# Kernel tuning notes

Hardware: AMD Instinct MI355X
Metric: run time of the kernel (lower is better)

The kernel has to match this reference:

```python
import jax, jax.numpy as jnp
import numpy as np

PATCH = (1, 5, 5)   # NN_patch_size (t, h, w)
CHUNK = 3600


def unfold3d_patches(video):
    """video: [B,C,T,H,W] -> [N, d] overlapping (1,5,5) patches, stride 1, VALID.
    d = C*1*5*5; N = B*T*(H-4)*(W-4). Element order within d is consistent
    across calls, which is all the L2 KNN + MSE math requires."""
    p = jax.lax.conv_general_dilated_patches(
        video, filter_shape=PATCH, window_strides=(1, 1, 1), padding='VALID')
    # p: [B, C*prod(PATCH), T', H', W']
    d = p.shape[1]
    return jnp.moveaxis(p, 1, -1).reshape(-1, d)


def knn_argmin(q, k):
    """Exact 1-NN under L2 (faiss IndexFlatL2 equivalent), chunked over queries."""
    kn = jnp.sum(k * k, axis=1)                      # [Nk]
    qc = q.reshape(-1, CHUNK, q.shape[1])            # [nchunks, CHUNK, d]

    def one_chunk(qb):
        qn = jnp.sum(qb * qb, axis=1, keepdims=True)  # [CHUNK,1]
        d2 = qn + kn[None, :] - 2.0 * (qb @ k.T)      # [CHUNK, Nk]
        return jnp.argmin(d2, axis=1)

    return jax.lax.map(one_chunk, qc).reshape(-1)    # [Nq]


def setup_inputs() -> dict:
    key = jax.random.key(0)
    k1, k2 = jax.random.split(key)
    shape = (1, 3, 4, 64, 64)  # [B,C,T,H,W]
    return {
        'result': jax.random.normal(k1, shape, dtype=jnp.float32),
        'valid_video': jax.random.normal(k2, shape, dtype=jnp.float32),
    }


def reference(result, valid_video):
    q = unfold3d_patches(result)        # [Nq, 75] query patches
    k = unfold3d_patches(valid_video)   # [Nk, 75] valid (key/value) patches
    idx = knn_argmin(q, k)              # [Nq] nearest valid patch per query
    nn = k[idx]                         # gather (F.embedding equivalent)
    # nn.MSELoss(reduction='sum')
    diff = q - nn
    return jnp.sum(diff * diff)
```

## Files before the change

### kernel.cpp

```cpp
#include <hip/hip_runtime.h>
#include <hip/hip_bf16.h>
#include <math.h>

typedef __attribute__((ext_vector_type(4))) float f32x4;
typedef __attribute__((ext_vector_type(2))) long long2_t;

#define NP 14400
#define NPK 14592
#define NSEG 16
#define NIT 57
#define GRPB 1536

__device__ __forceinline__ unsigned char f2fp8(float x) {
  unsigned u = __float_as_uint(x);
  unsigned sign = (u >> 31) << 7;
  int exp = (int)((u >> 23) & 0xFF) - 127;
  unsigned man = u & 0x7FFFFF;
  if (exp >= -6) {
    unsigned keep = man >> 20;
    unsigned rest = man & 0xFFFFF;
    keep += (rest > 0x80000u) || (rest == 0x80000u && (keep & 1));
    int e8 = exp + 7;
    if (keep == 8) { keep = 0; e8 += 1; }
    if (e8 > 15 || (e8 == 15 && keep == 7)) return sign | 0x7E;
    return sign | ((unsigned)e8 << 3) | keep;
  } else {
    float a = fabsf(x);
    int q = (int)(a * 512.f + 0.5f);
    if (q >= 8) return sign | 0x08;
    return sign | (unsigned)q;
  }
}
__device__ __forceinline__ float fp82f(unsigned char b) {
  unsigned e = (b >> 3) & 15, m = b & 7;
  float v = (e == 0) ? ldexpf((float)m, -9) : ldexpf((float)(8 + m), (int)e - 10);
  return (b & 0x80) ? -v : v;
}

__device__ __forceinline__ size_t f8idx(int p, int d) {
  int g = p >> 4, c = p & 15, ks = d >> 5, l4e = (d & 31) >> 3, e7 = d & 7;
  size_t base = (size_t)g * GRPB;
  if (ks < 2) return base + (size_t)((c + 16 * l4e) * 16 + ks * 8 + e7);
  return base + 1024 + (size_t)((c + 16 * l4e) * 8 + e7);
}

__global__ __launch_bounds__(256) void prep_kernel(
    const float* __restrict__ resv, const float* __restrict__ valv,
    unsigned char* __restrict__ Qb, unsigned char* __restrict__ Kb,
    float* __restrict__ qn, float* __restrict__ kn,
    unsigned* __restrict__ rminb) {
  int w = threadIdx.x >> 6;
  int lane = threadIdx.x & 63;
  int pg = blockIdx.x * 4 + w;
  int isK = pg >= NPK;
  int p = isK ? pg - NPK : pg;

  float v0 = 0.f, v1 = 0.f;
  if (p < NP) {
    const float* src = isK ? valv : resv;
    int t = p / 3600; int rem = p - t * 3600;
    int y = rem / 60;  int x = rem - y * 60;
    {
      int d = lane;
      int c = d / 25; int r = d - c * 25; int dy = r / 5; int dx = r - dy * 5;
      v0 = src[((c * 4 + t) * 64 + (y + dy)) * 64 + (x + dx)];
    }
    if (lane < 11) {
      int d = lane + 64;
      int c = d / 25; int r = d - c * 25; int dy = r / 5; int dx = r - dy * 5;
      v1 = src[((c * 4 + t) * 64 + (y + dy)) * 64 + (x + dx)];
    }
  }

  unsigned char b0, b1;
  if (isK) { b0 = f2fp8(v0); b1 = f2fp8(v1); }
  else     { b0 = f2fp8(-2.f * v0); b1 = f2fp8(-2.f * v1); }

  float sq;
  if (isK) {
    float d0 = fp82f(b0), d1 = fp82f(b1);
    sq = d0 * d0 + d1 * d1;
  } else {
    sq = v0 * v0 + v1 * v1;
  }
  #pragma unroll
  for (int off = 1; off < 64; off <<= 1) sq += __shfl_xor(sq, off, 64);

  unsigned char* dst = isK ? Kb : Qb;
  dst[f8idx(p, lane)] = b0;
  if (lane < 32) dst[f8idx(p, lane + 64)] = b1;
  if (lane == 0) {
    if (isK) kn[p] = (p < NP) ? sq : 3.39e38f;
    else { qn[p] = sq; rminb[p] = 0xFFFFFFFFu; }
  }
}

__global__ __launch_bounds__(64, 4) void knn_kernel(
    const unsigned char* __restrict__ Qb, const unsigned char* __restrict__ Kb,
    const float* __restrict__ kn, unsigned* __restrict__ rminb) {
  int b = blockIdx.x;
  int lin = (b & 7) * 456 + (b >> 3);
  int ns = lin / 228, rowblk = lin - ns * 228;
  int brow = rowblk * 64;
  int lane = threadIdx.x;
  int l15 = lane & 15, l4 = lane >> 4;

  const char* gW = (const char*)Kb + (size_t)(ns * NIT) * GRPB;
  const char* Aw = (const char*)Qb + (size_t)(rowblk * 4) * GRPB;
  int colbase = ns * 912 + l15;

  long af01[4][2]; long af2[4];
  #pragma unroll
  for (int rt = 0; rt < 4; ++rt) {
    long2_t t = *(const long2_t*)(Aw + rt * GRPB + lane * 16);
    af01[rt][0] = t[0]; af01[rt][1] = t[1];
    af2[rt] = *(const long*)(Aw + rt * GRPB + 1024 + lane * 8);
  }

  float rmin[4][4];
  #pragma unroll
  for (int rt = 0; rt < 4; ++rt)
    #pragma unroll
    for (int j = 0; j < 4; ++j) rmin[rt][j] = INFINITY;

  long2_t b01[2]; long b2[2]; float kvb[2];

  auto loadB = [&](int bi, int it) {
    const char* g = gW + (size_t)it * GRPB;
    b01[bi] = *(const long2_t*)(g + lane * 16);
    b2[bi]  = *(const long*)(g + 1024 + lane * 8);
    kvb[bi] = kn[colbase + it * 16];
  };

  auto compute = [&](int bi) {
    float kv = kvb[bi];
    f32x4 ci = {kv, kv, kv, kv};
    f32x4 acc[4];
    {
      long bv = b01[bi][0];
      #pragma unroll
      for (int rt = 0; rt < 4; ++rt)
        acc[rt] = __builtin_amdgcn_mfma_f32_16x16x32_fp8_fp8(
            af01[rt][0], bv, ci, 0, 0, 0);
    }
    {
      long bv = b01[bi][1];
      #pragma unroll
      for (int rt = 0; rt < 4; ++rt)
        acc[rt] = __builtin_amdgcn_mfma_f32_16x16x32_fp8_fp8(
            af01[rt][1], bv, acc[rt], 0, 0, 0);
    }
    {
      long bv = b2[bi];
      #pragma unroll
      for (int rt = 0; rt < 4; ++rt)
        acc[rt] = __builtin_amdgcn_mfma_f32_16x16x32_fp8_fp8(
            af2[rt], bv, acc[rt], 0, 0, 0);
    }
    #pragma unroll
    for (int rt = 0; rt < 4; ++rt)
      #pragma unroll
      for (int j = 0; j < 4; ++j)
        rmin[rt][j] = fminf(rmin[rt][j], acc[rt][j]);
  };

  loadB(0, 0);
  loadB(1, 1);

  int k = 0;
  #pragma unroll 1
  for (int tri = 0; tri < 27; ++tri, k += 2) {
    compute(0); loadB(0, k + 2);
    compute(1); loadB(1, k + 3);
  }
  compute(0); loadB(0, 56);
  compute(1);
  compute(0);

  #pragma unroll
  for (int rt = 0; rt < 4; ++rt)
    #pragma unroll
    for (int j = 0; j < 4; ++j) {
      float m = rmin[rt][j];
      m = fminf(m, __shfl_xor(m, 1, 64));
      m = fminf(m, __shfl_xor(m, 2, 64));
      m = fminf(m, __shfl_xor(m, 4, 64));
      m = fminf(m, __shfl_xor(m, 8, 64));
      if (l15 == 0) {
        unsigned bu = __float_as_uint(m);
        unsigned tu = bu ^ (unsigned)(((int)bu >> 31) | (int)0x80000000);
        atomicMin(&rminb[brow + rt * 16 + l4 * 4 + j], tu);
      }
    }
}

__global__ __launch_bounds__(64) void final1_kernel(
    const unsigned* __restrict__ rminb, const float* __restrict__ qn,
    float* __restrict__ partial) {
  int r = blockIdx.x * 64 + threadIdx.x;
  unsigned u = rminb[r];
  unsigned bu = (u & 0x80000000u) ? (u ^ 0x80000000u) : ~u;
  float val = __uint_as_float(bu) + qn[r];
  #pragma unroll
  for (int off = 32; off; off >>= 1) val += __shfl_down(val, off, 64);
  if (threadIdx.x == 0) partial[blockIdx.x] = val;
}

__global__ __launch_bounds__(256) void final2_kernel(
    const float* __restrict__ partial, float* __restrict__ out) {
  int t = threadIdx.x;
  float v = (t < 225) ? partial[t] : 0.f;
  #pragma unroll
  for (int off = 32; off; off >>= 1) v += __shfl_down(v, off, 64);
  __shared__ float s[4];
  if ((t & 63) == 0) s[t >> 6] = v;
  __syncthreads();
  if (t == 0) out[0] = s[0] + s[1] + s[2] + s[3];
}

extern "C" void kernel_launch(void* const* d_in, const int* in_sizes, int n_in,
                              void* d_out, int out_size, void* d_ws, size_t ws_size,
                              hipStream_t stream) {
  const float* resv = (const float*)d_in[0];
  const float* valv = (const float*)d_in[1];
  char* ws = (char*)d_ws;
  unsigned char* Qb = (unsigned char*)ws;
  unsigned char* Kb = (unsigned char*)(ws + 1400832);
  float* qn         = (float*)(ws + 2801664);
  float* kn         = (float*)(ws + 2860032);
  unsigned* rminb   = (unsigned*)(ws + 2918400);
  float* partial    = (float*)(ws + 2976768);
  float* out = (float*)d_out;

  prep_kernel<<<7296, 256, 0, stream>>>(resv, valv, Qb, Kb, qn, kn, rminb);
  knn_kernel<<<3648, 64, 0, stream>>>(Qb, Kb, kn, rminb);
  final1_kernel<<<225, 64, 0, stream>>>(rminb, qn, partial);
  final2_kernel<<<1, 256, 0, stream>>>(partial, out);
}
```

Measured before the change: 49.44 us.

## Use 16x16x128 scaled fp8 MFMA with padded 128-wide patch layout; merge final reductions

Replaces three 16x16x32 fp8 MFMAs per tile with one gfx950 scaled 16x16x128 f8f6f4 MFMA, padding the patch dimension to 128 bytes. The operand layout changes to 32 contiguous bytes per lane, so each fragment is a single 32-byte load and the prep kernel zero-fills the padding. The two final reduction kernels are merged into one 1024-thread kernel to save a launch. The padding raises the fp8 workspace traffic from 96 to 128 bytes per patch, and the neutral scale value (0x7F) must leave the products unchanged.

```diff
diff --git a/kernel.cpp b/kernel.cpp
--- a/kernel.cpp
+++ b/kernel.cpp
@@ -1,15 +1,14 @@
 #include <hip/hip_runtime.h>
-#include <hip/hip_bf16.h>
 #include <math.h>
 
 typedef __attribute__((ext_vector_type(4))) float f32x4;
-typedef __attribute__((ext_vector_type(2))) long long2_t;
+typedef __attribute__((ext_vector_type(8))) int int8v;
 
 #define NP 14400
 #define NPK 14592
 #define NSEG 16
 #define NIT 57
-#define GRPB 1536
+#define GRPB 2048
 
 __device__ __forceinline__ unsigned char f2fp8(float x) {
   unsigned u = __float_as_uint(x);
@@ -38,10 +37,8 @@
 }
 
 __device__ __forceinline__ size_t f8idx(int p, int d) {
-  int g = p >> 4, c = p & 15, ks = d >> 5, l4e = (d & 31) >> 3, e7 = d & 7;
-  size_t base = (size_t)g * GRPB;
-  if (ks < 2) return base + (size_t)((c + 16 * l4e) * 16 + ks * 8 + e7);
-  return base + 1024 + (size_t)((c + 16 * l4e) * 8 + e7);
+  return (size_t)(p >> 4) * GRPB
+       + (size_t)((((p & 15) + 16 * (d >> 5)) * 32) + (d & 31));
 }
 
 __global__ __launch_bounds__(256) void prep_kernel(
@@ -88,7 +85,12 @@
 
   unsigned char* dst = isK ? Kb : Qb;
   dst[f8idx(p, lane)] = b0;
-  if (lane < 32) dst[f8idx(p, lane + 64)] = b1;
+  if (lane < 32) {
+    dst[f8idx(p, lane + 64)] = b1;
+  } else {
+    dst[(size_t)(p >> 4) * GRPB
+        + (size_t)((((p & 15) + 48) * 32) + (lane - 32))] = 0;
+  }
   if (lane == 0) {
     if (isK) kn[p] = (p < NP) ? sq : 3.39e38f;
     else { qn[p] = sq; rminb[p] = 0xFFFFFFFFu; }
@@ -105,17 +107,14 @@
   int lane = threadIdx.x;
   int l15 = lane & 15, l4 = lane >> 4;
 
-  const char* gW = (const char*)Kb + (size_t)(ns * NIT) * GRPB;
-  const char* Aw = (const char*)Qb + (size_t)(rowblk * 4) * GRPB;
+  const char* gW = (const char*)Kb + (size_t)(ns * NIT) * GRPB + lane * 32;
+  const char* Aw = (const char*)Qb + (size_t)(rowblk * 4) * GRPB + lane * 32;
   int colbase = ns * 912 + l15;
 
-  long af01[4][2]; long af2[4];
-  #pragma unroll
-  for (int rt = 0; rt < 4; ++rt) {
-    long2_t t = *(const long2_t*)(Aw + rt * GRPB + lane * 16);
-    af01[rt][0] = t[0]; af01[rt][1] = t[1];
-    af2[rt] = *(const long*)(Aw + rt * GRPB + 1024 + lane * 8);
-  }
+  int8v af[4];
+  #pragma unroll
+  for (int rt = 0; rt < 4; ++rt)
+    af[rt] = *(const int8v*)(Aw + rt * GRPB);
 
   float rmin[4][4];
   #pragma unroll
@@ -123,12 +122,10 @@
     #pragma unroll
     for (int j = 0; j < 4; ++j) rmin[rt][j] = INFINITY;
 
-  long2_t b01[2]; long b2[2]; float kvb[2];
+  int8v bbuf[2]; float kvb[2];
 
   auto loadB = [&](int bi, int it) {
-    const char* g = gW + (size_t)it * GRPB;
-    b01[bi] = *(const long2_t*)(g + lane * 16);
-    b2[bi]  = *(const long*)(g + 1024 + lane * 8);
+    bbuf[bi] = *(const int8v*)(gW + (size_t)it * GRPB);
     kvb[bi] = kn[colbase + it * 16];
   };
 
@@ -136,27 +133,11 @@
     float kv = kvb[bi];
     f32x4 ci = {kv, kv, kv, kv};
     f32x4 acc[4];
-    {
-      long bv = b01[bi][0];
-      #pragma unroll
-      for (int rt = 0; rt < 4; ++rt)
-        acc[rt] = __builtin_amdgcn_mfma_f32_16x16x32_fp8_fp8(
-            af01[rt][0], bv, ci, 0, 0, 0);
-    }
-    {
-      long bv = b01[bi][1];
-      #pragma unroll
-      for (int rt = 0; rt < 4; ++rt)
-        acc[rt] = __builtin_amdgcn_mfma_f32_16x16x32_fp8_fp8(
-            af01[rt][1], bv, acc[rt], 0, 0, 0);
-    }
-    {
-      long bv = b2[bi];
-      #pragma unroll
-      for (int rt = 0; rt < 4; ++rt)
-        acc[rt] = __builtin_amdgcn_mfma_f32_16x16x32_fp8_fp8(
-            af2[rt], bv, acc[rt], 0, 0, 0);
-    }
+    #pragma unroll
+    for (int rt = 0; rt < 4; ++rt)
+      acc[rt] = __builtin_amdgcn_mfma_scale_f32_16x16x128_f8f6f4(
+          af[rt], bbuf[bi], ci, 0, 0,
+          0, 0x7F7F7F7F, 0, 0x7F7F7F7F);
     #pragma unroll
     for (int rt = 0; rt < 4; ++rt)
       #pragma unroll
@@ -194,28 +175,27 @@
     }
 }
 
-__global__ __launch_bounds__(64) void final1_kernel(
+__global__ __launch_bounds__(1024) void final_kernel(
     const unsigned* __restrict__ rminb, const float* __restrict__ qn,
-    float* __restrict__ partial) {
-  int r = blockIdx.x * 64 + threadIdx.x;
-  unsigned u = rminb[r];
-  unsigned bu = (u & 0x80000000u) ? (u ^ 0x80000000u) : ~u;
-  float val = __uint_as_float(bu) + qn[r];
-  #pragma unroll
-  for (int off = 32; off; off >>= 1) val += __shfl_down(val, off, 64);
-  if (threadIdx.x == 0) partial[blockIdx.x] = val;
-}
-
-__global__ __launch_bounds__(256) void final2_kernel(
-    const float* __restrict__ partial, float* __restrict__ out) {
+    float* __restrict__ out) {
   int t = threadIdx.x;
-  float v = (t < 225) ? partial[t] : 0.f;
-  #pragma unroll
-  for (int off = 32; off; off >>= 1) v += __shfl_down(v, off, 64);
-  __shared__ float s[4];
-  if ((t & 63) == 0) s[t >> 6] = v;
+  float s = 0.f;
+  for (int i = t; i < NP; i += 1024) {
+    unsigned u = rminb[i];
+    unsigned bu = (u & 0x80000000u) ? (u ^ 0x80000000u) : ~u;
+    s += __uint_as_float(bu) + qn[i];
+  }
+  #pragma unroll
+  for (int off = 32; off; off >>= 1) s += __shfl_down(s, off, 64);
+  __shared__ float red[16];
+  if ((t & 63) == 0) red[t >> 6] = s;
   __syncthreads();
-  if (t == 0) out[0] = s[0] + s[1] + s[2] + s[3];
+  if (t == 0) {
+    float tot = 0.f;
+    #pragma unroll
+    for (int i2 = 0; i2 < 16; ++i2) tot += red[i2];
+    out[0] = tot;
+  }
 }
 
 extern "C" void kernel_launch(void* const* d_in, const int* in_sizes, int n_in,
@@ -225,15 +205,13 @@
   const float* valv = (const float*)d_in[1];
   char* ws = (char*)d_ws;
   unsigned char* Qb = (unsigned char*)ws;
-  unsigned char* Kb = (unsigned char*)(ws + 1400832);
-  float* qn         = (float*)(ws + 2801664);
-  float* kn         = (float*)(ws + 2860032);
-  unsigned* rminb   = (unsigned*)(ws + 2918400);
-  float* partial    = (float*)(ws + 2976768);
+  unsigned char* Kb = (unsigned char*)(ws + 1867776);
+  float* qn         = (float*)(ws + 3735552);
+  float* kn         = (float*)(ws + 3793920);
+  unsigned* rminb   = (unsigned*)(ws + 3852288);
   float* out = (float*)d_out;
 
   prep_kernel<<<7296, 256, 0, stream>>>(resv, valv, Qb, Kb, qn, kn, rminb);
   knn_kernel<<<3648, 64, 0, stream>>>(Qb, Kb, kn, rminb);
-  final1_kernel<<<225, 64, 0, stream>>>(rminb, qn, partial);
-  final2_kernel<<<1, 256, 0, stream>>>(partial, out);
-}
+  final_kernel<<<1, 1024, 0, stream>>>(rminb, qn, out);
+}
```

Result: faster. 46.59 us (-5.8%).
